# Kernel tuning notes

Measured on AMD Instinct MI355X. Metric: run time of the kernel, lower is better.

Reference implementation:

```python
import jax, jax.numpy as jnp
import numpy as np

E = 1024
M = 6
GH = 256
FR = 16  # FiLM bottleneck r = max(16, E//64)


def setup_inputs() -> dict:
    key = jax.random.key(0)
    ks = jax.random.split(key, 32)
    n = lambda k, shape, std=0.02: jax.random.normal(k, shape, dtype=jnp.float32) * std
    inp = {
        "x": jax.random.normal(ks[0], (4, 2048, E), dtype=jnp.float32),
        # gate MLP E->GH->M
        "gw1": n(ks[1], (E, GH)), "gb1": jnp.zeros((GH,), jnp.float32),
        "gw2": n(ks[2], (GH, M)), "gb2": jnp.zeros((M,), jnp.float32),
        "ebias": jnp.zeros((M,), jnp.float32),
        "pm_alpha": jnp.float32(0.5),
        # expert 0: DoubleMLP E->2E->E
        "dfc_w": n(ks[3], (E, 2 * E)), "dfc_b": jnp.zeros((2 * E,), jnp.float32),
        "dproj_w": n(ks[4], (2 * E, E)), "dproj_b": jnp.zeros((E,), jnp.float32),
        # expert 1: SingleMLP E->E->E
        "sfc_w": n(ks[5], (E, E)), "sfc_b": jnp.zeros((E,), jnp.float32),
        "sproj_w": n(ks[6], (E, E)), "sproj_b": jnp.zeros((E,), jnp.float32),
        # expert 2: rank-2 perceptron
        "p2_w": n(ks[7], (2, E)), "p2_v": n(ks[8], (2, E)),
        "p2_alpha": jnp.ones((2,), jnp.float32), "p2_b": jnp.zeros((2,), jnp.float32),
        "p2_bias": jnp.zeros((E,), jnp.float32),
        # expert 3: rank-4 perceptron
        "p4_w": n(ks[9], (4, E)), "p4_v": n(ks[10], (4, E)),
        "p4_alpha": jnp.ones((4,), jnp.float32), "p4_b": jnp.zeros((4,), jnp.float32),
        "p4_bias": jnp.zeros((E,), jnp.float32),
        # expert 4: ReGLU1D
        "rg_u": n(ks[11], (E,)), "rg_a": jnp.ones((E,), jnp.float32),
        "rg_b": jnp.zeros((1,), jnp.float32), "rg_bias": jnp.zeros((E,), jnp.float32),
        # expert 5: FiLM E->FR->2E
        "fl_dw": n(ks[12], (E, FR)), "fl_db": jnp.zeros((FR,), jnp.float32),
        "fl_uw": n(ks[13], (FR, 2 * E)), "fl_ub": jnp.zeros((2 * E,), jnp.float32),
    }
    return inp


def _gelu(x):
    return jax.nn.gelu(x, approximate=False)  # torch nn.GELU default (erf)


def _rank_n(x, w, v, alpha, b, biasvec):
    # y = biasvec + sum_i alpha_i * gelu(<w_i,x> + b_i) * v_i
    s = jnp.einsum("bse,ne->bsn", x, w) + b
    g = _gelu(s)
    return jnp.einsum("bsn,ne->bse", alpha * g, v) + biasvec


def reference(x, gw1, gb1, gw2, gb2, ebias, pm_alpha,
              dfc_w, dfc_b, dproj_w, dproj_b,
              sfc_w, sfc_b, sproj_w, sproj_b,
              p2_w, p2_v, p2_alpha, p2_b, p2_bias,
              p4_w, p4_v, p4_alpha, p4_b, p4_bias,
              rg_u, rg_a, rg_b, rg_bias,
              fl_dw, fl_db, fl_uw, fl_ub):
    # gate logits [B,S,M]; tau=1.0
    gl = _gelu(x @ gw1 + gb1) @ gw2 + gb2 + ebias
    pi = jax.nn.softmax(gl, axis=-1)
    # top_k=1 sparse weights: mask to top-1 then renormalize
    _, topi = jax.lax.top_k(pi, 1)
    mask = jax.nn.one_hot(topi[..., 0], M, dtype=pi.dtype)
    w = pi * mask
    w = w / (jnp.sum(w, axis=-1, keepdims=True) + 1e-9)

    # experts (dropout = identity in eval)
    o0 = _gelu(x @ dfc_w + dfc_b) @ dproj_w + dproj_b            # DoubleMLP
    o1 = _gelu(x @ sfc_w + sfc_b) @ sproj_w + sproj_b            # SingleMLP
    o2 = _rank_n(x, p2_w, p2_v, p2_alpha, p2_b, p2_bias)          # perc2
    o3 = _rank_n(x, p4_w, p4_v, p4_alpha, p4_b, p4_bias)          # perc4
    s = x @ rg_u + rg_b[0]                                        # ReGLU1D
    o4 = jax.nn.sigmoid(s)[..., None] * (x * rg_a) + rg_bias
    t = _gelu(x @ fl_dw + fl_db)                                  # FiLM
    gb = t @ fl_uw + fl_ub
    gamma, beta = jnp.split(gb, 2, axis=-1)
    o5 = gamma * x + beta

    all_out = jnp.stack([o0, o1, o2, o3, o4, o5], axis=-1)        # [B,S,E,M]
    mixed = jnp.sum(all_out * w[..., None, :], axis=-1)
    return pm_alpha * mixed
```

## Files before the change

### kernel.cpp

```cpp
#include <hip/hip_runtime.h>
#include <math.h>


#define E 1024
#define GH 256
#define NEXP 6
#define NTOK 8192
#define NCH 24

typedef __attribute__((ext_vector_type(8))) short bf16x8;
typedef __attribute__((ext_vector_type(4))) float f32x4;

__device__ __forceinline__ float gelu_erf(float v) {
    return 0.5f * v * (1.0f + erff(v * 0.70710678118654752440f));
}

__device__ __forceinline__ unsigned short f2bf(float f) {
    union { float f; unsigned u; } c; c.f = f;
    unsigned u = c.u;
    u += 0x7fffu + ((u >> 16) & 1u);
    return (unsigned short)(u >> 16);
}

__device__ __forceinline__ float bf2f(unsigned short h) {
    union { unsigned u; float f; } c; c.u = ((unsigned)h) << 16;
    return c.f;
}

__device__ __forceinline__ int ldso(int row, int q) {
    return row * 32 + ((q ^ ((row >> 1) & 3)) << 3);
}

__device__ __forceinline__ void glds16(const void* g, void* l) {
    __builtin_amdgcn_global_load_lds(
        (const __attribute__((address_space(1))) void*)g,
        (__attribute__((address_space(3))) void*)l, 16, 0, 0);
}

__global__ __launch_bounds__(256)
void prep_kernel(const float* __restrict__ x, unsigned short* __restrict__ xh,
                 unsigned short* __restrict__ xl,
                 const float* __restrict__ gw1, unsigned short* __restrict__ w1cat,
                 const float* __restrict__ p2_w, const float* __restrict__ p4_w,
                 const float* __restrict__ rg_u, const float* __restrict__ fl_dw,
                 unsigned short* __restrict__ w1cheap,
                 const float* __restrict__ p2_bias, const float* __restrict__ p2_v,
                 const float* __restrict__ p4_bias, const float* __restrict__ p4_v,
                 const float* __restrict__ rg_a, const float* __restrict__ rg_bias,
                 const float* __restrict__ fl_uw, const float* __restrict__ fl_ub,
                 unsigned short* __restrict__ bta, unsigned short* __restrict__ btm,
                 const float* __restrict__ dfc_w, unsigned short* __restrict__ dfc_wt,
                 const float* __restrict__ dproj_w, unsigned short* __restrict__ dpj_wt,
                 const float* __restrict__ sfc_w, unsigned short* __restrict__ sfc_wt,
                 const float* __restrict__ sproj_w, unsigned short* __restrict__ spj_wt) {
    __shared__ float tile[32][33];
    const int tid = threadIdx.x;
    const int tx = tid & 31, ty = tid >> 5;
    int b = blockIdx.x;
    if (b < 2048) {
        const int n4 = NTOK * E / 4;
        for (int i = b * 256 + tid; i < n4; i += 2048 * 256) {
            float4 v = reinterpret_cast<const float4*>(x)[i];
            ushort4 h, l;
            h.x = f2bf(v.x); l.x = f2bf(v.x - bf2f(h.x));
            h.y = f2bf(v.y); l.y = f2bf(v.y - bf2f(h.y));
            h.z = f2bf(v.z); l.z = f2bf(v.z - bf2f(h.z));
            h.w = f2bf(v.w); l.w = f2bf(v.w - bf2f(h.w));
            reinterpret_cast<ushort4*>(xh)[i] = h;
            reinterpret_cast<ushort4*>(xl)[i] = l;
        }
        return;
    }
    b -= 2048;
    if (b < 256) {
        const int c0 = (b & 7) * 32, r0 = (b >> 3) * 32;
#pragma unroll
        for (int i = 0; i < 4; ++i)
            tile[ty + i * 8][tx] = gw1[(size_t)(r0 + ty + i * 8) * GH + c0 + tx];
        __syncthreads();
#pragma unroll
        for (int i = 0; i < 4; ++i) {
            float v = tile[tx][ty + i * 8];
            unsigned short h = f2bf(v);
            size_t row = (size_t)(c0 + ty + i * 8) * 2048;
            w1cat[row + r0 + tx] = h;
            w1cat[row + 1024 + r0 + tx] = f2bf(v - bf2f(h));
        }
        return;
    }
    b -= 256;
    if (b < 64) {
        const int r = b;
        const int k4 = tid * 4;
        float4 v = {0.f, 0.f, 0.f, 0.f};
        if (r < 2)       v = *reinterpret_cast<const float4*>(&p2_w[r * E + k4]);
        else if (r < 6)  v = *reinterpret_cast<const float4*>(&p4_w[(r - 2) * E + k4]);
        else if (r == 6) v = *reinterpret_cast<const float4*>(&rg_u[k4]);
        else if (r < 23) {
            const int j = r - 7;
            v.x = fl_dw[(k4 + 0) * 16 + j];
            v.y = fl_dw[(k4 + 1) * 16 + j];
            v.z = fl_dw[(k4 + 2) * 16 + j];
            v.w = fl_dw[(k4 + 3) * 16 + j];
        }
        ushort4 h, l;
        h.x = f2bf(v.x); l.x = f2bf(v.x - bf2f(h.x));
        h.y = f2bf(v.y); l.y = f2bf(v.y - bf2f(h.y));
        h.z = f2bf(v.z); l.z = f2bf(v.z - bf2f(h.z));
        h.w = f2bf(v.w); l.w = f2bf(v.w - bf2f(h.w));
        *reinterpret_cast<ushort4*>(&w1cheap[r * 2048 + k4]) = h;
        *reinterpret_cast<ushort4*>(&w1cheap[r * 2048 + 1024 + k4]) = l;
        return;
    }
    b -= 64;
    if (b < 4) {
        const int n = b * 256 + tid;
        float av[32], mv[32];
#pragma unroll
        for (int r = 0; r < 32; ++r) { av[r] = 0.f; mv[r] = 0.f; }
        av[0] = p2_bias[n];
        av[1] = p2_v[n]; av[2] = p2_v[E + n];
        av[3] = p4_bias[n];
#pragma unroll
        for (int j = 0; j < 4; ++j) av[4 + j] = p4_v[j * E + n];
        av[8] = rg_bias[n];
        mv[9] = rg_a[n];
        av[10] = fl_ub[E + n];
        mv[10] = fl_ub[n];
#pragma unroll
        for (int j = 0; j < 16; ++j) {
            av[11 + j] = fl_uw[(size_t)j * 2 * E + E + n];
            mv[11 + j] = fl_uw[(size_t)j * 2 * E + n];
        }
#pragma unroll
        for (int r = 0; r < 32; ++r) {
            unsigned short ha = f2bf(av[r]), hm = f2bf(mv[r]);
            bta[n * 64 + r] = ha; bta[n * 64 + 32 + r] = ha;
            btm[n * 64 + r] = hm; btm[n * 64 + 32 + r] = hm;
        }
        return;
    }
    b -= 4;
    const float* src; unsigned short* dst; int R, C, nbx;
    if (b < 2048)      { src = dfc_w;   dst = dfc_wt; R = 1024; C = 2048; nbx = 64; }
    else if (b < 4096) { src = dproj_w; dst = dpj_wt; R = 2048; C = 1024; nbx = 32; b -= 2048; }
    else if (b < 5120) { src = sfc_w;   dst = sfc_wt; R = 1024; C = 1024; nbx = 32; b -= 4096; }
    else               { src = sproj_w; dst = spj_wt; R = 1024; C = 1024; nbx = 32; b -= 5120; }
    const int c0 = (b % nbx) * 32, r0 = (b / nbx) * 32;
#pragma unroll
    for (int i = 0; i < 4; ++i)
        tile[ty + i * 8][tx] = src[(size_t)(r0 + ty + i * 8) * C + c0 + tx];
    __syncthreads();
#pragma unroll
    for (int i = 0; i < 4; ++i)
        dst[(size_t)(c0 + ty + i * 8) * R + r0 + tx] = f2bf(tile[tx][ty + i * 8]);
}

__global__ __launch_bounds__(256)
void gate_partial_kernel(const unsigned short* __restrict__ xh,
                         const unsigned short* __restrict__ xl,
                         const unsigned short* __restrict__ w1cat,
                         const unsigned short* __restrict__ w1cheap,
                         float* __restrict__ hp,
                         float* __restrict__ cdot) {
    __shared__ __align__(16) unsigned short As[2][128 * 64];
    __shared__ __align__(16) unsigned short Bs[2][128 * 64];
    const int tid = threadIdx.x;
    const int bid = blockIdx.x;
    const int xcd = bid & 7, slot = bid >> 3;
    const int nx = slot & 1;
    const int strip = xcd * 32 + (slot >> 1);
    const int m = strip >> 2, c2 = strip & 3;
    const int z = c2 & 1, h = c2 >> 1;
    const int t0 = m * 128, n0 = nx * 128;
    const unsigned short* A = z ? xl : xh;
    float* hpz = hp + (size_t)c2 * ((size_t)NTOK * GH);
    float* cd  = cdot + (size_t)c2 * ((size_t)NTOK * NCH);

    const int lane = tid & 63, wv = tid >> 6;
    const int wr = wv >> 1, wc = wv & 1;
    const int lm = lane & 15, q = lane >> 4;
    const int r0 = tid >> 2, gsl = tid & 3;
    const int g = gsl ^ ((r0 >> 1) & 3);
    const int lbase = wv * 512;

    const unsigned short* pa0 = A + (size_t)(t0 + r0) * E + g * 8;
    const unsigned short* pa1 = A + (size_t)(t0 + 64 + r0) * E + g * 8;
    const unsigned short* pb0 = w1cat + (size_t)(n0 + r0) * 2048 + h * 1024 + g * 8;
    const unsigned short* pb1 = w1cat + (size_t)(n0 + 64 + r0) * 2048 + h * 1024 + g * 8;
    const unsigned short* pcw = w1cheap + (size_t)(nx * 16 + lm) * 2048 + h * 1024 + q * 8;

    f32x4 acc[4][4];
#pragma unroll
    for (int s = 0; s < 4; ++s)
#pragma unroll
        for (int t = 0; t < 4; ++t) acc[s][t] = (f32x4){0.f, 0.f, 0.f, 0.f};
    f32x4 accC[2];
    accC[0] = (f32x4){0.f, 0.f, 0.f, 0.f};
    accC[1] = (f32x4){0.f, 0.f, 0.f, 0.f};

    glds16(pa0, &As[0][lbase]);
    glds16(pa1, &As[0][2048 + lbase]);
    glds16(pa0 + 32, &As[0][4096 + lbase]);
    glds16(pa1 + 32, &As[0][4096 + 2048 + lbase]);
    glds16(pb0, &Bs[0][lbase]);
    glds16(pb1, &Bs[0][2048 + lbase]);
    glds16(pb0 + 32, &Bs[0][4096 + lbase]);
    glds16(pb1 + 32, &Bs[0][4096 + 2048 + lbase]);
    bf16x8 cf0 = *(const bf16x8*)pcw;
    bf16x8 cf1 = *(const bf16x8*)(pcw + 32);

    int cur = 0;
    for (int k0 = 0;; k0 += 64) {
        __syncthreads();
        const int kn = k0 + 64;
        bf16x8 cf0n, cf1n;
        if (kn < 1024) {
            glds16(pa0 + kn, &As[cur ^ 1][lbase]);
            glds16(pa1 + kn, &As[cur ^ 1][2048 + lbase]);
            glds16(pa0 + kn + 32, &As[cur ^ 1][4096 + lbase]);
            glds16(pa1 + kn + 32, &As[cur ^ 1][4096 + 2048 + lbase]);
            glds16(pb0 + kn, &Bs[cur ^ 1][lbase]);
            glds16(pb1 + kn, &Bs[cur ^ 1][2048 + lbase]);
            glds16(pb0 + kn + 32, &Bs[cur ^ 1][4096 + lbase]);
            glds16(pb1 + kn + 32, &Bs[cur ^ 1][4096 + 2048 + lbase]);
            cf0n = *(const bf16x8*)(pcw + kn);
            cf1n = *(const bf16x8*)(pcw + kn + 32);
        }
#pragma unroll
        for (int sub = 0; sub < 2; ++sub) {
            const int off = sub * 4096;
            bf16x8 af[4], bfr[4];
#pragma unroll
            for (int s = 0; s < 4; ++s) af[s] = *(const bf16x8*)&As[cur][off + ldso(wr * 64 + s * 16 + lm, q)];
#pragma unroll
            for (int t = 0; t < 4; ++t) bfr[t] = *(const bf16x8*)&Bs[cur][off + ldso(wc * 64 + t * 16 + lm, q)];
#pragma unroll
            for (int s = 0; s < 4; ++s)
#pragma unroll
                for (int t = 0; t < 4; ++t)
                    acc[s][t] = __builtin_amdgcn_mfma_f32_16x16x32_bf16(af[s], bfr[t], acc[s][t], 0, 0, 0);
            bf16x8 cf = sub ? cf1 : cf0;
            bf16x8 ac0 = wc ? af[2] : af[0];
            bf16x8 ac1 = wc ? af[3] : af[1];
            accC[0] = __builtin_amdgcn_mfma_f32_16x16x32_bf16(ac0, cf, accC[0], 0, 0, 0);
            accC[1] = __builtin_amdgcn_mfma_f32_16x16x32_bf16(ac1, cf, accC[1], 0, 0, 0);
        }
        if (kn >= 1024) break;
        cf0 = cf0n; cf1 = cf1n; cur ^= 1;
    }
#pragma unroll
    for (int s = 0; s < 4; ++s)
#pragma unroll
        for (int t = 0; t < 4; ++t)
#pragma unroll
            for (int rg = 0; rg < 4; ++rg) {
                int rl = wr * 64 + s * 16 + q * 4 + rg;
                int c  = wc * 64 + t * 16 + lm;
                hpz[(size_t)(t0 + rl) * GH + n0 + c] = acc[s][t][rg];
            }
    const int cc = nx * 16 + lm;
    if (cc < NCH) {
#pragma unroll
        for (int i = 0; i < 2; ++i)
#pragma unroll
            for (int rg = 0; rg < 4; ++rg) {
                int rl = wr * 64 + wc * 32 + i * 16 + q * 4 + rg;
                cd[(size_t)(t0 + rl) * NCH + cc] = accC[i][rg];
            }
    }
}

__global__ __launch_bounds__(256)
void gate_finalize_kernel(const float* __restrict__ hp,
                          const float* __restrict__ gb1, const float* __restrict__ gw2,
                          const float* __restrict__ gb2, const float* __restrict__ ebias,
                          const float* __restrict__ pm_alpha,
                          const float* __restrict__ cdot,
                          const float* __restrict__ p2_alpha, const float* __restrict__ p2_b,
                          const float* __restrict__ p4_alpha, const float* __restrict__ p4_b,
                          const float* __restrict__ rg_b, const float* __restrict__ fl_db,
                          float* __restrict__ scale, int* __restrict__ counts,
                          int* __restrict__ tlist,
                          unsigned short* __restrict__ Cm) {
    __shared__ float hs[32][264];
    __shared__ float g2s[GH * NEXP];
    __shared__ int tokexp[32];
    const int tid = threadIdx.x;
    const int t0 = blockIdx.x * 32;
    const size_t HPS = (size_t)NTOK * GH;
    for (int i = tid; i < GH * NEXP; i += 256) g2s[i] = gw2[i];
#pragma unroll
    for (int i = 0; i < 8; ++i) {
        int f4 = i * 256 + tid;
        int row = f4 >> 6, c4 = (f4 & 63) * 4;
        size_t base = (size_t)(t0 + row) * GH + c4;
        float4 a = *reinterpret_cast<const float4*>(&hp[base]);
        float4 b = *reinterpret_cast<const float4*>(&hp[HPS + base]);
        float4 c = *reinterpret_cast<const float4*>(&hp[2 * HPS + base]);
        float4 d = *reinterpret_cast<const float4*>(&hp[3 * HPS + base]);
        float4 o;
        o.x = gelu_erf(a.x + b.x + c.x + d.x + gb1[c4 + 0]);
        o.y = gelu_erf(a.y + b.y + c.y + d.y + gb1[c4 + 1]);
        o.z = gelu_erf(a.z + b.z + c.z + d.z + gb1[c4 + 2]);
        o.w = gelu_erf(a.w + b.w + c.w + d.w + gb1[c4 + 3]);
        *reinterpret_cast<float4*>(&hs[row][c4]) = o;
    }
    __syncthreads();
    const int t = tid >> 3, j = tid & 7;
    float p[NEXP] = {0.f, 0.f, 0.f, 0.f, 0.f, 0.f};
#pragma unroll 8
    for (int kk = 0; kk < 32; ++kk) {
        int k = j + kk * 8;
        float hv = hs[t][k];
        const float* gr = &g2s[k * NEXP];
#pragma unroll
        for (int m = 0; m < NEXP; ++m) p[m] += hv * gr[m];
    }
#pragma unroll
    for (int m = 0; m < NEXP; ++m) {
        p[m] += __shfl_xor(p[m], 4, 64);
        p[m] += __shfl_xor(p[m], 2, 64);
        p[m] += __shfl_xor(p[m], 1, 64);
    }
    if (j == 0) {
        float L[NEXP];
#pragma unroll
        for (int m = 0; m < NEXP; ++m) L[m] = p[m] + gb2[m] + ebias[m];
        float mx = L[0]; int am = 0;
#pragma unroll
        for (int m = 1; m < NEXP; ++m) { if (L[m] > mx) { mx = L[m]; am = m; } }
        float S = 0.f;
#pragma unroll
        for (int m = 0; m < NEXP; ++m) S += expf(L[m] - mx);
        float pt = 1.f / S;
        scale[t0 + t] = pm_alpha[0] * (pt / (pt + 1e-9f));
        tokexp[t] = am;
    }
    __syncthreads();
    if (tid < NEXP) {
        const int e = tid;
        int cnt = 0;
#pragma unroll
        for (int i = 0; i < 32; ++i) cnt += (tokexp[i] == e);
        if (cnt) {
            int base = atomicAdd(&counts[e], cnt);
            int pos = 0;
#pragma unroll
            for (int i = 0; i < 32; ++i)
                if (tokexp[i] == e) tlist[e * NTOK + base + (pos++)] = t0 + i;
        }
    }
    const size_t CDS = (size_t)NTOK * NCH;
    for (int i = tid; i < 32 * 32; i += 256) {
        const int tt = i >> 5, r = i & 31;
        const int tok = t0 + tt;
        const int e = tokexp[tt];
        float c = 0.f;
        int slot = -1;
        if (r == 0)       { if (e == 2) c = 1.f; }
        else if (r <= 2)  { if (e == 2) slot = r - 1; }
        else if (r == 3)  { if (e == 3) c = 1.f; }
        else if (r <= 7)  { if (e == 3) slot = r - 2; }
        else if (r == 8)  { if (e == 4) c = 1.f; }
        else if (r == 9)  { if (e == 4) slot = 6; }
        else if (r == 10) { if (e == 5) c = 1.f; }
        else if (r <= 26) { if (e == 5) slot = r - 4; }
        if (slot >= 0) {
            size_t idx = (size_t)tok * NCH + slot;
            float s = cdot[idx] + cdot[CDS + idx] + cdot[2 * CDS + idx] + cdot[3 * CDS + idx];
            if (slot < 2)       c = p2_alpha[slot] * gelu_erf(s + p2_b[slot]);
            else if (slot < 6)  c = p4_alpha[slot - 2] * gelu_erf(s + p4_b[slot - 2]);
            else if (slot == 6) c = 1.f / (1.f + expf(-(s + rg_b[0])));
            else                c = gelu_erf(s + fl_db[slot - 7]);
        }
        unsigned short hi = f2bf(c);
        Cm[(size_t)tok * 64 + r] = hi;
        Cm[(size_t)tok * 64 + 32 + r] = f2bf(c - bf2f(hi));
    }
}

#define STAGEAB(t, jb)                                            \
    do {                                                          \
        glds16(pa + (t) * 64,      &As[jb][lbase]);               \
        glds16(pa + (t) * 64 + 32, &As[jb][2048 + lbase]);        \
        glds16(pb + (t) * 64,      &Bs[jb][lbase]);               \
        glds16(pb + (t) * 64 + 32, &Bs[jb][2048 + lbase]);        \
    } while (0)

__global__ __launch_bounds__(256)
void moe_gemm1_kernel(const unsigned short* __restrict__ xh,
                      const unsigned short* __restrict__ B0, const unsigned short* __restrict__ B1,
                      const float* __restrict__ bias0, const float* __restrict__ bias1,
                      const int* __restrict__ counts, const int* __restrict__ tlist,
                      unsigned short* __restrict__ H0, unsigned short* __restrict__ H1,
                      const unsigned short* __restrict__ Cm,
                      const unsigned short* __restrict__ bta, const unsigned short* __restrict__ btm,
                      const float* __restrict__ x, const float* __restrict__ scale,
                      float* __restrict__ out) {
    __shared__ __align__(16) unsigned short As[3][64 * 64];
    __shared__ __align__(16) unsigned short Bs[3][64 * 64];
    __shared__ int toks[64];
    const int tid = threadIdx.x;
    const int bid = blockIdx.x;
    const int lane = tid & 63, wv = tid >> 6;
    const int wm = (wv & 1) * 32, wn = (wv >> 1) * 32;
    const int lm = lane & 15, q = lane >> 4;
    const int r0 = tid >> 2, gsl = tid & 3;
    const int g = gsl ^ ((r0 >> 1) & 3);
    const int lbase = wv * 512;

    if (bid >= 2048) {
        const int cg = bid - 2048;
        const int xcd = cg & 7, s = cg >> 3;
        const int nx = s & 15;
        const int mt = xcd + 8 * (s >> 4);
        const int t0 = mt * 64, n0 = nx * 64;
        unsigned short* Ct = &As[0][0];
        unsigned short* Ba = &As[1][0];
        unsigned short* Bm = &As[2][0];

        const unsigned short* pc = Cm + (size_t)(t0 + r0) * 64 + g * 8;
        const unsigned short* pba = bta + (size_t)(n0 + r0) * 64 + g * 8;
        const unsigned short* pbm = btm + (size_t)(n0 + r0) * 64 + g * 8;
        glds16(pc,       &Ct[lbase]);
        glds16(pc + 32,  &Ct[2048 + lbase]);
        glds16(pba,      &Ba[lbase]);
        glds16(pba + 32, &Ba[2048 + lbase]);
        glds16(pbm,      &Bm[lbase]);
        glds16(pbm + 32, &Bm[2048 + lbase]);

        f32x4 accA[2][2], accM[2][2];
#pragma unroll
        for (int s2 = 0; s2 < 2; ++s2)
#pragma unroll
            for (int t2 = 0; t2 < 2; ++t2) {
                accA[s2][t2] = (f32x4){0.f, 0.f, 0.f, 0.f};
                accM[s2][t2] = (f32x4){0.f, 0.f, 0.f, 0.f};
            }
        __syncthreads();
#pragma unroll
        for (int sub = 0; sub < 2; ++sub) {
            const int off = sub * 2048;
            bf16x8 af[2], ba[2], bm[2];
#pragma unroll
            for (int s2 = 0; s2 < 2; ++s2) af[s2] = *(const bf16x8*)&Ct[off + ldso(wm + s2 * 16 + lm, q)];
#pragma unroll
            for (int t2 = 0; t2 < 2; ++t2) {
                ba[t2] = *(const bf16x8*)&Ba[off + ldso(wn + t2 * 16 + lm, q)];
                bm[t2] = *(const bf16x8*)&Bm[off + ldso(wn + t2 * 16 + lm, q)];
            }
#pragma unroll
            for (int s2 = 0; s2 < 2; ++s2)
#pragma unroll
                for (int t2 = 0; t2 < 2; ++t2) {
                    accA[s2][t2] = __builtin_amdgcn_mfma_f32_16x16x32_bf16(af[s2], ba[t2], accA[s2][t2], 0, 0, 0);
                    accM[s2][t2] = __builtin_amdgcn_mfma_f32_16x16x32_bf16(af[s2], bm[t2], accM[s2][t2], 0, 0, 0);
                }
        }
#pragma unroll
        for (int s2 = 0; s2 < 2; ++s2)
#pragma unroll
            for (int t2 = 0; t2 < 2; ++t2)
#pragma unroll
                for (int rg = 0; rg < 4; ++rg) {
                    int rl = wm + s2 * 16 + q * 4 + rg;
                    int gc = n0 + wn + t2 * 16 + lm;
                    int tok = t0 + rl;
                    float xv = x[(size_t)tok * E + gc];
                    out[(size_t)tok * E + gc] =
                        scale[tok] * (accM[s2][t2][rg] * xv + accA[s2][t2][rg]);
                }
        return;
    }

    const int xcd = bid & 7, slot = bid >> 3;
    const int nx = slot & 31;
    const int strip = xcd + 8 * (slot >> 5);
    const int z = strip & 1;
    const int N = z ? 1024 : 2048;
    const int cnt = counts[z];
    const int i0 = (strip >> 1) * 64;
    const int n0 = nx * 64;
    if (i0 >= cnt || n0 >= N) return;
    const unsigned short* Bz = z ? B1 : B0;
    const float* bias = z ? bias1 : bias0;

    if (tid < 64) toks[tid] = tlist[z * NTOK + min(i0 + tid, cnt - 1)];
    __syncthreads();

    const unsigned short* pa = xh + (size_t)toks[r0] * E + g * 8;
    const unsigned short* pb = Bz + (size_t)(n0 + r0) * E + g * 8;

    f32x4 acc[2][2];
#pragma unroll
    for (int s = 0; s < 2; ++s)
#pragma unroll
        for (int t = 0; t < 2; ++t) acc[s][t] = (f32x4){0.f, 0.f, 0.f, 0.f};

    STAGEAB(0, 0); STAGEAB(1, 1); STAGEAB(2, 2);

    const int nt = E / 64;
    for (int i = 0; i < nt; ++i) {
        const int ahead = nt - 1 - i;
        if (ahead >= 2)      asm volatile("s_waitcnt vmcnt(8)" ::: "memory");
        else if (ahead == 1) asm volatile("s_waitcnt vmcnt(4)" ::: "memory");
        else                 asm volatile("s_waitcnt vmcnt(0)" ::: "memory");
        asm volatile("s_barrier" ::: "memory");
        const int jb = i % 3;
#pragma unroll
        for (int sub = 0; sub < 2; ++sub) {
            const int off = sub * 2048;
            bf16x8 af[2], bfr[2];
#pragma unroll
            for (int s = 0; s < 2; ++s) af[s] = *(const bf16x8*)&As[jb][off + ldso(wm + s * 16 + lm, q)];
#pragma unroll
            for (int t = 0; t < 2; ++t) bfr[t] = *(const bf16x8*)&Bs[jb][off + ldso(wn + t * 16 + lm, q)];
#pragma unroll
            for (int s = 0; s < 2; ++s)
#pragma unroll
                for (int t = 0; t < 2; ++t)
                    acc[s][t] = __builtin_amdgcn_mfma_f32_16x16x32_bf16(af[s], bfr[t], acc[s][t], 0, 0, 0);
        }
        asm volatile("s_barrier" ::: "memory");
        if (i + 3 < nt) STAGEAB(i + 3, jb);
    }
    unsigned short* Hz = z ? H1 : H0;
#pragma unroll
    for (int s = 0; s < 2; ++s)
#pragma unroll
        for (int t = 0; t < 2; ++t)
#pragma unroll
            for (int rg = 0; rg < 4; ++rg) {
                int rl = wm + s * 16 + q * 4 + rg;
                int gc = n0 + wn + t * 16 + lm;
                float v = acc[s][t][rg] + bias[gc];
                Hz[(size_t)(i0 + rl) * N + gc] = f2bf(gelu_erf(v));
            }
}

__global__ __launch_bounds__(256)
void moe_gemm2_kernel(const unsigned short* __restrict__ h1, const unsigned short* __restrict__ h2,
                      const unsigned short* __restrict__ dpj, const unsigned short* __restrict__ spj,
                      const float* __restrict__ dproj_b, const float* __restrict__ sproj_b,
                      const int* __restrict__ counts, const int* __restrict__ tlist,
                      const float* __restrict__ scale,
                      float* __restrict__ out) {
    __shared__ __align__(16) unsigned short As[3][64 * 64];
    __shared__ __align__(16) unsigned short Bs[3][64 * 64];
    __shared__ int toks[64];
    const int tid = threadIdx.x;
    const int bb = blockIdx.x;
    const int lane = tid & 63;

    const int xcd = bb & 7, slot = bb >> 3;
    const int nx = slot & 15;
    const int strip = xcd + 8 * (slot >> 4);
    const int z = strip & 1;
    const int i0 = (strip >> 1) * 64;
    const int n0 = nx * 64;
    const int K = z ? 1024 : 2048;
    const int cnt = counts[z];
    if (i0 >= cnt) return;
    const int rows = min(64, cnt - i0);
    const unsigned short* Az = z ? h2 : h1;
    const unsigned short* Bz = z ? spj : dpj;
    const float* bias = z ? sproj_b : dproj_b;

    if (tid < 64) toks[tid] = tlist[z * NTOK + min(i0 + tid, cnt - 1)];
    __syncthreads();

    const int wv = tid >> 6;
    const int wm = (wv & 1) * 32, wn = (wv >> 1) * 32;
    const int lm = lane & 15, q = lane >> 4;
    const int r0 = tid >> 2, gsl = tid & 3;
    const int g = gsl ^ ((r0 >> 1) & 3);
    const int lbase = wv * 512;

    const unsigned short* pa = Az + (size_t)(i0 + r0) * K + g * 8;
    const unsigned short* pb = Bz + (size_t)(n0 + r0) * K + g * 8;

    f32x4 acc[2][2];
#pragma unroll
    for (int s = 0; s < 2; ++s)
#pragma unroll
        for (int t = 0; t < 2; ++t) acc[s][t] = (f32x4){0.f, 0.f, 0.f, 0.f};

    STAGEAB(0, 0); STAGEAB(1, 1); STAGEAB(2, 2);

    const int nt = K / 64;
    for (int i = 0; i < nt; ++i) {
        const int ahead = nt - 1 - i;
        if (ahead >= 2)      asm volatile("s_waitcnt vmcnt(8)" ::: "memory");
        else if (ahead == 1) asm volatile("s_waitcnt vmcnt(4)" ::: "memory");
        else                 asm volatile("s_waitcnt vmcnt(0)" ::: "memory");
        asm volatile("s_barrier" ::: "memory");
        const int jb = i % 3;
#pragma unroll
        for (int sub = 0; sub < 2; ++sub) {
            const int off = sub * 2048;
            bf16x8 af[2], bfr[2];
#pragma unroll
            for (int s = 0; s < 2; ++s) af[s] = *(const bf16x8*)&As[jb][off + ldso(wm + s * 16 + lm, q)];
#pragma unroll
            for (int t = 0; t < 2; ++t) bfr[t] = *(const bf16x8*)&Bs[jb][off + ldso(wn + t * 16 + lm, q)];
#pragma unroll
            for (int s = 0; s < 2; ++s)
#pragma unroll
                for (int t = 0; t < 2; ++t)
                    acc[s][t] = __builtin_amdgcn_mfma_f32_16x16x32_bf16(af[s], bfr[t], acc[s][t], 0, 0, 0);
        }
        asm volatile("s_barrier" ::: "memory");
        if (i + 3 < nt) STAGEAB(i + 3, jb);
    }
#pragma unroll
    for (int s = 0; s < 2; ++s)
#pragma unroll
        for (int t = 0; t < 2; ++t)
#pragma unroll
            for (int rg = 0; rg < 4; ++rg) {
                int rl = wm + s * 16 + q * 4 + rg;
                if (rl < rows) {
                    int gc = n0 + wn + t * 16 + lm;
                    int tok = toks[rl];
                    out[(size_t)tok * E + gc] = scale[tok] * (acc[s][t][rg] + bias[gc]);
                }
            }
}

extern "C" void kernel_launch(void* const* d_in, const int* in_sizes, int n_in,
                              void* d_out, int out_size, void* d_ws, size_t ws_size,
                              hipStream_t stream) {
    const float* x        = (const float*)d_in[0];
    const float* gw1      = (const float*)d_in[1];
    const float* gb1      = (const float*)d_in[2];
    const float* gw2      = (const float*)d_in[3];
    const float* gb2      = (const float*)d_in[4];
    const float* ebias    = (const float*)d_in[5];
    const float* pm_alpha = (const float*)d_in[6];
    const float* dfc_w    = (const float*)d_in[7];
    const float* dfc_b    = (const float*)d_in[8];
    const float* dproj_w  = (const float*)d_in[9];
    const float* dproj_b  = (const float*)d_in[10];
    const float* sfc_w    = (const float*)d_in[11];
    const float* sfc_b    = (const float*)d_in[12];
    const float* sproj_w  = (const float*)d_in[13];
    const float* sproj_b  = (const float*)d_in[14];
    const float* p2_w     = (const float*)d_in[15];
    const float* p2_v     = (const float*)d_in[16];
    const float* p2_alpha = (const float*)d_in[17];
    const float* p2_b     = (const float*)d_in[18];
    const float* p2_bias  = (const float*)d_in[19];
    const float* p4_w     = (const float*)d_in[20];
    const float* p4_v     = (const float*)d_in[21];
    const float* p4_alpha = (const float*)d_in[22];
    const float* p4_b     = (const float*)d_in[23];
    const float* p4_bias  = (const float*)d_in[24];
    const float* rg_u     = (const float*)d_in[25];
    const float* rg_a     = (const float*)d_in[26];
    const float* rg_b     = (const float*)d_in[27];
    const float* rg_bias  = (const float*)d_in[28];
    const float* fl_dw    = (const float*)d_in[29];
    const float* fl_db    = (const float*)d_in[30];
    const float* fl_uw    = (const float*)d_in[31];
    const float* fl_ub    = (const float*)d_in[32];
    float* out = (float*)d_out;

    char* ws = (char*)d_ws;
    size_t off = 0;
    int*            counts = (int*)(ws + off);            off += 256;
    float*          scale  = (float*)(ws + off);          off += (size_t)NTOK * 4;
    int*            tlist  = (int*)(ws + off);            off += (size_t)NEXP * NTOK * 4;
    float*          cdot   = (float*)(ws + off);          off += (size_t)4 * NTOK * NCH * 4;
    unsigned short* Cm     = (unsigned short*)(ws + off); off += (size_t)NTOK * 64 * 2;
    unsigned short* bta    = (unsigned short*)(ws + off); off += (size_t)E * 64 * 2;
    unsigned short* btm    = (unsigned short*)(ws + off); off += (size_t)E * 64 * 2;
    unsigned short* w1cheap= (unsigned short*)(ws + off); off += (size_t)64 * 2048 * 2;
    unsigned short* w1cat  = (unsigned short*)(ws + off); off += (size_t)GH * 2048 * 2;
    unsigned short* dfc_wt = (unsigned short*)(ws + off); off += (size_t)2048 * 1024 * 2;
    unsigned short* dpj_wt = (unsigned short*)(ws + off); off += (size_t)1024 * 2048 * 2;
    unsigned short* sfc_wt = (unsigned short*)(ws + off); off += (size_t)1024 * 1024 * 2;
    unsigned short* spj_wt = (unsigned short*)(ws + off); off += (size_t)1024 * 1024 * 2;
    unsigned short* x_hi   = (unsigned short*)(ws + off); off += (size_t)NTOK * E * 2;
    char* U = ws + off;
    unsigned short* x_lo = (unsigned short*)U;
    unsigned short* h1   = (unsigned short*)U;
    unsigned short* h2   = (unsigned short*)(U + (size_t)16 * 1024 * 1024);
    float* hp = out;

    hipMemsetAsync(counts, 0, 256, stream);
    prep_kernel<<<8516, 256, 0, stream>>>(x, x_hi, x_lo, gw1, w1cat,
                                          p2_w, p4_w, rg_u, fl_dw, w1cheap,
                                          p2_bias, p2_v, p4_bias, p4_v,
                                          rg_a, rg_bias, fl_uw, fl_ub, bta, btm,
                                          dfc_w, dfc_wt, dproj_w, dpj_wt,
                                          sfc_w, sfc_wt, sproj_w, spj_wt);
    gate_partial_kernel<<<512, 256, 0, stream>>>(
        x_hi, x_lo, w1cat, w1cheap, hp, cdot);
    gate_finalize_kernel<<<NTOK / 32, 256, 0, stream>>>(
        hp, gb1, gw2, gb2, ebias, pm_alpha, cdot,
        p2_alpha, p2_b, p4_alpha, p4_b, rg_b, fl_db,
        scale, counts, tlist, Cm);
    moe_gemm1_kernel<<<4096, 256, 0, stream>>>(
        x_hi, dfc_wt, sfc_wt, dfc_b, sfc_b, counts, tlist, h1, h2,
        Cm, bta, btm, x, scale, out);
    moe_gemm2_kernel<<<1024, 256, 0, stream>>>(
        h1, h2, dpj_wt, spj_wt, dproj_b, sproj_b, counts, tlist, scale, out);
    (void)in_sizes; (void)n_in; (void)out_size; (void)ws_size;
}
```

Measured before the change: 260.2 us.

## Drop lo×lo gate partial product and switch gate GEMM to 3-stage pipeline

The gate GEMM used a split-bf16 (hi/lo) decomposition with four partial products (xh·Wh, xl·Wh, xh·Wl, xl·Wl); this drops the xl·Wl term, leaving three partials. The grid shrinks from 512 to 384 blocks and the finalize kernels sum three partials instead of four. The K loop is also restructured into a 3-stage triple-buffered pipeline with 32-wide K tiles, explicit vmcnt waits and raw barriers, replacing the double-buffered 64-wide loop. The dropped term is a second-order precision correction, so gate logits lose a little accuracy, which could flip top-1 routing in near-tie cases.

```diff
diff --git a/kernel.cpp b/kernel.cpp
--- a/kernel.cpp
+++ b/kernel.cpp
@@ -163,14 +163,14 @@
                          const unsigned short* __restrict__ w1cheap,
                          float* __restrict__ hp,
                          float* __restrict__ cdot) {
-    __shared__ __align__(16) unsigned short As[2][128 * 64];
-    __shared__ __align__(16) unsigned short Bs[2][128 * 64];
+    __shared__ __align__(16) unsigned short As[3][128 * 32];
+    __shared__ __align__(16) unsigned short Bs[3][128 * 32];
     const int tid = threadIdx.x;
     const int bid = blockIdx.x;
     const int xcd = bid & 7, slot = bid >> 3;
     const int nx = slot & 1;
-    const int strip = xcd * 32 + (slot >> 1);
-    const int m = strip >> 2, c2 = strip & 3;
+    const int idx = xcd * 24 + (slot >> 1);
+    const int m = idx / 3, c2 = idx - 3 * m;
     const int z = c2 & 1, h = c2 >> 1;
     const int t0 = m * 128, n0 = nx * 128;
     const unsigned short* A = z ? xl : xh;
@@ -199,56 +199,51 @@
     accC[0] = (f32x4){0.f, 0.f, 0.f, 0.f};
     accC[1] = (f32x4){0.f, 0.f, 0.f, 0.f};
 
-    glds16(pa0, &As[0][lbase]);
-    glds16(pa1, &As[0][2048 + lbase]);
-    glds16(pa0 + 32, &As[0][4096 + lbase]);
-    glds16(pa1 + 32, &As[0][4096 + 2048 + lbase]);
-    glds16(pb0, &Bs[0][lbase]);
-    glds16(pb1, &Bs[0][2048 + lbase]);
-    glds16(pb0 + 32, &Bs[0][4096 + lbase]);
-    glds16(pb1 + 32, &Bs[0][4096 + 2048 + lbase]);
-    bf16x8 cf0 = *(const bf16x8*)pcw;
-    bf16x8 cf1 = *(const bf16x8*)(pcw + 32);
-
-    int cur = 0;
-    for (int k0 = 0;; k0 += 64) {
-        __syncthreads();
-        const int kn = k0 + 64;
-        bf16x8 cf0n, cf1n;
-        if (kn < 1024) {
-            glds16(pa0 + kn, &As[cur ^ 1][lbase]);
-            glds16(pa1 + kn, &As[cur ^ 1][2048 + lbase]);
-            glds16(pa0 + kn + 32, &As[cur ^ 1][4096 + lbase]);
-            glds16(pa1 + kn + 32, &As[cur ^ 1][4096 + 2048 + lbase]);
-            glds16(pb0 + kn, &Bs[cur ^ 1][lbase]);
-            glds16(pb1 + kn, &Bs[cur ^ 1][2048 + lbase]);
-            glds16(pb0 + kn + 32, &Bs[cur ^ 1][4096 + lbase]);
-            glds16(pb1 + kn + 32, &Bs[cur ^ 1][4096 + 2048 + lbase]);
-            cf0n = *(const bf16x8*)(pcw + kn);
-            cf1n = *(const bf16x8*)(pcw + kn + 32);
-        }
-#pragma unroll
-        for (int sub = 0; sub < 2; ++sub) {
-            const int off = sub * 4096;
-            bf16x8 af[4], bfr[4];
-#pragma unroll
-            for (int s = 0; s < 4; ++s) af[s] = *(const bf16x8*)&As[cur][off + ldso(wr * 64 + s * 16 + lm, q)];
-#pragma unroll
-            for (int t = 0; t < 4; ++t) bfr[t] = *(const bf16x8*)&Bs[cur][off + ldso(wc * 64 + t * 16 + lm, q)];
-#pragma unroll
-            for (int s = 0; s < 4; ++s)
-#pragma unroll
-                for (int t = 0; t < 4; ++t)
-                    acc[s][t] = __builtin_amdgcn_mfma_f32_16x16x32_bf16(af[s], bfr[t], acc[s][t], 0, 0, 0);
-            bf16x8 cf = sub ? cf1 : cf0;
+#define GSTAGE(t, jb)                                            \
+    do {                                                         \
+        glds16(pa0 + (t) * 32, &As[jb][lbase]);                  \
+        glds16(pa1 + (t) * 32, &As[jb][2048 + lbase]);           \
+        glds16(pb0 + (t) * 32, &Bs[jb][lbase]);                  \
+        glds16(pb1 + (t) * 32, &Bs[jb][2048 + lbase]);           \
+    } while (0)
+
+    GSTAGE(0, 0); bf16x8 cfA = *(const bf16x8*)(pcw);
+    GSTAGE(1, 1); bf16x8 cfB = *(const bf16x8*)(pcw + 32);
+    GSTAGE(2, 2); bf16x8 cfC = *(const bf16x8*)(pcw + 64);
+
+    const int nt = 32;
+    for (int i = 0; i < nt; ++i) {
+        const int ahead = nt - 1 - i;
+        if (ahead >= 2)      asm volatile("s_waitcnt vmcnt(10)" ::: "memory");
+        else if (ahead == 1) asm volatile("s_waitcnt vmcnt(5)" ::: "memory");
+        else                 asm volatile("s_waitcnt vmcnt(0)" ::: "memory");
+        asm volatile("s_barrier" ::: "memory");
+        const int jb = i % 3;
+        bf16x8 af[4], bfr[4];
+#pragma unroll
+        for (int s = 0; s < 4; ++s) af[s] = *(const bf16x8*)&As[jb][ldso(wr * 64 + s * 16 + lm, q)];
+#pragma unroll
+        for (int t = 0; t < 4; ++t) bfr[t] = *(const bf16x8*)&Bs[jb][ldso(wc * 64 + t * 16 + lm, q)];
+#pragma unroll
+        for (int s = 0; s < 4; ++s)
+#pragma unroll
+            for (int t = 0; t < 4; ++t)
+                acc[s][t] = __builtin_amdgcn_mfma_f32_16x16x32_bf16(af[s], bfr[t], acc[s][t], 0, 0, 0);
+        {
             bf16x8 ac0 = wc ? af[2] : af[0];
             bf16x8 ac1 = wc ? af[3] : af[1];
-            accC[0] = __builtin_amdgcn_mfma_f32_16x16x32_bf16(ac0, cf, accC[0], 0, 0, 0);
-            accC[1] = __builtin_amdgcn_mfma_f32_16x16x32_bf16(ac1, cf, accC[1], 0, 0, 0);
-        }
-        if (kn >= 1024) break;
-        cf0 = cf0n; cf1 = cf1n; cur ^= 1;
-    }
+            accC[0] = __builtin_amdgcn_mfma_f32_16x16x32_bf16(ac0, cfA, accC[0], 0, 0, 0);
+            accC[1] = __builtin_amdgcn_mfma_f32_16x16x32_bf16(ac1, cfA, accC[1], 0, 0, 0);
+        }
+        asm volatile("s_barrier" ::: "memory");
+        bf16x8 cfn = cfA;
+        if (i + 3 < nt) {
+            GSTAGE(i + 3, jb);
+            cfn = *(const bf16x8*)(pcw + (i + 3) * 32);
+        }
+        cfA = cfB; cfB = cfC; cfC = cfn;
+    }
+#undef GSTAGE
 #pragma unroll
     for (int s = 0; s < 4; ++s)
 #pragma unroll
@@ -298,12 +293,11 @@
         float4 a = *reinterpret_cast<const float4*>(&hp[base]);
         float4 b = *reinterpret_cast<const float4*>(&hp[HPS + base]);
         float4 c = *reinterpret_cast<const float4*>(&hp[2 * HPS + base]);
-        float4 d = *reinterpret_cast<const float4*>(&hp[3 * HPS + base]);
         float4 o;
-        o.x = gelu_erf(a.x + b.x + c.x + d.x + gb1[c4 + 0]);
-        o.y = gelu_erf(a.y + b.y + c.y + d.y + gb1[c4 + 1]);
-        o.z = gelu_erf(a.z + b.z + c.z + d.z + gb1[c4 + 2]);
-        o.w = gelu_erf(a.w + b.w + c.w + d.w + gb1[c4 + 3]);
+        o.x = gelu_erf(a.x + b.x + c.x + gb1[c4 + 0]);
+        o.y = gelu_erf(a.y + b.y + c.y + gb1[c4 + 1]);
+        o.z = gelu_erf(a.z + b.z + c.z + gb1[c4 + 2]);
+        o.w = gelu_erf(a.w + b.w + c.w + gb1[c4 + 3]);
         *reinterpret_cast<float4*>(&hs[row][c4]) = o;
     }
     __syncthreads();
@@ -368,7 +362,7 @@
         else if (r <= 26) { if (e == 5) slot = r - 4; }
         if (slot >= 0) {
             size_t idx = (size_t)tok * NCH + slot;
-            float s = cdot[idx] + cdot[CDS + idx] + cdot[2 * CDS + idx] + cdot[3 * CDS + idx];
+            float s = cdot[idx] + cdot[CDS + idx] + cdot[2 * CDS + idx];
             if (slot < 2)       c = p2_alpha[slot] * gelu_erf(s + p2_b[slot]);
             else if (slot < 6)  c = p4_alpha[slot - 2] * gelu_erf(s + p4_b[slot - 2]);
             else if (slot == 6) c = 1.f / (1.f + expf(-(s + rg_b[0])));
@@ -671,7 +665,7 @@
     int*            counts = (int*)(ws + off);            off += 256;
     float*          scale  = (float*)(ws + off);          off += (size_t)NTOK * 4;
     int*            tlist  = (int*)(ws + off);            off += (size_t)NEXP * NTOK * 4;
-    float*          cdot   = (float*)(ws + off);          off += (size_t)4 * NTOK * NCH * 4;
+    float*          cdot   = (float*)(ws + off);          off += (size_t)3 * NTOK * NCH * 4;
     unsigned short* Cm     = (unsigned short*)(ws + off); off += (size_t)NTOK * 64 * 2;
     unsigned short* bta    = (unsigned short*)(ws + off); off += (size_t)E * 64 * 2;
     unsigned short* btm    = (unsigned short*)(ws + off); off += (size_t)E * 64 * 2;
@@ -695,7 +689,7 @@
                                           rg_a, rg_bias, fl_uw, fl_ub, bta, btm,
                                           dfc_w, dfc_wt, dproj_w, dpj_wt,
                                           sfc_w, sfc_wt, sproj_w, spj_wt);
-    gate_partial_kernel<<<512, 256, 0, stream>>>(
+    gate_partial_kernel<<<384, 256, 0, stream>>>(
         x_hi, x_lo, w1cat, w1cheap, hp, cdot);
     gate_finalize_kernel<<<NTOK / 32, 256, 0, stream>>>(
         hp, gb1, gw2, gb2, ebias, pm_alpha, cdot,
```

Result: no change. 265.4 us (+2.0%).
